# Kernel optimization log

Hardware: AMD Instinct MI355X
Metric: run time of the kernel (lower is better)

Reference implementation:

```python
import jax, jax.numpy as jnp
import numpy as np

N, E, IN_DIM, OUT_DIM, R = 50000, 800000, 128, 128, 8


def setup_inputs() -> dict:
    key = jax.random.key(0)
    k1, k2, k3, k4, k5 = jax.random.split(key, 5)
    x = jax.random.normal(k1, (N, IN_DIM), dtype=jnp.float32)
    edge_index = jax.random.randint(k2, (2, E), 0, N, dtype=jnp.int32)
    edge_type = jax.random.randint(k3, (E,), 0, R, dtype=jnp.int32)
    # Xavier-uniform-ish init for parameters
    lim_w = float(np.sqrt(6.0 / (IN_DIM + OUT_DIM)))
    weight = jax.random.uniform(k4, (R, IN_DIM, OUT_DIM), dtype=jnp.float32, minval=-lim_w, maxval=lim_w)
    self_weight = jax.random.uniform(k5, (IN_DIM, OUT_DIM), dtype=jnp.float32, minval=-lim_w, maxval=lim_w)
    return {"x": x, "weight": weight, "self_weight": self_weight,
            "edge_index": edge_index, "edge_type": edge_type}


def reference(x, weight, self_weight, edge_index, edge_type):
    n = x.shape[0]
    r = weight.shape[0]
    d_out = weight.shape[2]
    src, dst = edge_index[0], edge_index[1]
    # undirected: symmetrize edges (directed=False)
    src_all = jnp.concatenate([src, dst])          # [2E]
    dst_all = jnp.concatenate([dst, src])          # [2E]
    et_all = jnp.concatenate([edge_type, edge_type])  # [2E]
    # transform all nodes by every relation weight once: [R, N, D_out]
    xw = jnp.einsum('ni,rio->rno', x, weight)
    # gather per-edge messages already transformed by their relation's W_r
    msg = xw[et_all, src_all]                      # [2E, D_out]
    # fused (relation, dst) segment id -> per-relation scatter-add
    seg = et_all.astype(jnp.int32) * n + dst_all
    agg = jax.ops.segment_sum(msg, seg, num_segments=r * n).reshape(r, n, d_out)
    deg = jax.ops.segment_sum(jnp.ones_like(seg, dtype=x.dtype), seg,
                              num_segments=r * n).reshape(r, n)
    deg_inv = jnp.where(deg > 0, 1.0 / jnp.maximum(deg, 1.0), jnp.zeros_like(deg))
    out = jnp.sum(agg * deg_inv[..., None], axis=0)  # [N, D_out]
    out = out + x @ self_weight                       # self-loop
    return out
```

## Files before the change

kernel.cpp:

```cpp
#include <hip/hip_runtime.h>

#define NN 50000
#define EE 800000
#define RR 8
#define DD 128
#define SS (NN*RR)
#define TE (2*EE)
#define NB 782
#define NBLK 391
#define NS (NB*NBLK)
#define CONVB 6826
#define XWB 391

typedef __attribute__((ext_vector_type(8))) short bf16x8;
typedef __attribute__((ext_vector_type(4))) float f32x4;

#define DRAIN_VM do { \
    asm volatile("s_waitcnt vmcnt(0)" ::: "memory"); \
    __builtin_amdgcn_sched_barrier(0); \
  } while (0)

__device__ __forceinline__ unsigned short f2bf(float f){
  unsigned int u = __float_as_uint(f);
  u += 0x7fffu + ((u >> 16) & 1u);
  return (unsigned short)(u >> 16);
}
__device__ __forceinline__ float bf_lo(unsigned int w){ return __uint_as_float(w << 16); }
__device__ __forceinline__ float bf_hi(unsigned int w){ return __uint_as_float(w & 0xffff0000u); }

__device__ __forceinline__ void acc8(float* a, uint4 u){
  a[0] += bf_lo(u.x); a[1] += bf_hi(u.x);
  a[2] += bf_lo(u.y); a[3] += bf_hi(u.y);
  a[4] += bf_lo(u.z); a[5] += bf_hi(u.z);
  a[6] += bf_lo(u.w); a[7] += bf_hi(u.w);
}
__device__ __forceinline__ void acc8s(float* a, uint4 u, float s){
  a[0] += s*bf_lo(u.x); a[1] += s*bf_hi(u.x);
  a[2] += s*bf_lo(u.y); a[3] += s*bf_hi(u.y);
  a[4] += s*bf_lo(u.z); a[5] += s*bf_hi(u.z);
  a[6] += s*bf_lo(u.w); a[7] += s*bf_hi(u.w);
}

__device__ __forceinline__ void dir_edge(const int* ei, const int* et, int j,
                                         int& s, int& d, int& t){
  if (j < EE){ s = ei[j]; d = ei[EE + j]; t = et[j]; }
  else { int jj = j - EE; s = ei[EE + jj]; d = ei[jj]; t = et[jj]; }
}

__global__ __launch_bounds__(256) void k_histconv(
    const int* __restrict__ ei, const int* __restrict__ et,
    int* __restrict__ hist,
    const float* __restrict__ x, const float* __restrict__ w,
    const float* __restrict__ sw,
    unsigned short* __restrict__ xb, unsigned short* __restrict__ wb)
{
  __shared__ int h[NB];
  if (blockIdx.x < NBLK){
    int tid = threadIdx.x, bid = blockIdx.x;
    for (int i = tid; i < NB; i += 256) h[i] = 0;
    __syncthreads();
    int j0 = bid*4096;
    for (int k = tid; k < 4096; k += 256){
      int j = j0 + k;
      if (j < TE){
        int d = (j < EE) ? ei[EE + j] : ei[j - EE];
        atomicAdd(&h[d >> 6], 1);
      }
    }
    __syncthreads();
    for (int i = tid; i < NB; i += 256) hist[i*NBLK + bid] = h[i];
  } else {
    int i = (blockIdx.x - NBLK)*256 + threadIdx.x;
    const int M1 = NN*DD/4;
    if (i < M1){
      float4 v = ((const float4*)x)[i];
      ushort4 o;
      o.x = f2bf(v.x); o.y = f2bf(v.y); o.z = f2bf(v.z); o.w = f2bf(v.w);
      ((ushort4*)xb)[i] = o;
    } else {
      int j = i - M1;
      if (j < 9*DD*DD){
        int r = j >> 14; int rem = j & 16383; int n = rem >> 7; int k = rem & 127;
        float v = (r < 8) ? w[r*16384 + k*128 + n] : sw[k*128 + n];
        wb[j] = f2bf(v);
      }
    }
  }
}

__global__ __launch_bounds__(256) void k_scan1(int* __restrict__ hist,
                                               int* __restrict__ blksum){
  __shared__ int sd[256];
  int b = blockIdx.x, tid = threadIdx.x;
  int base = b*1024 + tid*4;
  int v0 = (base+0 < NS) ? hist[base+0] : 0;
  int v1 = (base+1 < NS) ? hist[base+1] : 0;
  int v2 = (base+2 < NS) ? hist[base+2] : 0;
  int v3 = (base+3 < NS) ? hist[base+3] : 0;
  int ts = v0+v1+v2+v3;
  sd[tid] = ts; __syncthreads();
  for (int o = 1; o < 256; o <<= 1){
    int t = (tid >= o) ? sd[tid-o] : 0;
    __syncthreads();
    sd[tid] += t;
    __syncthreads();
  }
  int ex = sd[tid] - ts;
  if (base+0 < NS) hist[base+0] = ex; ex += v0;
  if (base+1 < NS) hist[base+1] = ex; ex += v1;
  if (base+2 < NS) hist[base+2] = ex; ex += v2;
  if (base+3 < NS) hist[base+3] = ex;
  if (tid == 255) blksum[b] = sd[255];
}

__global__ __launch_bounds__(256) void k_scan3(int* __restrict__ hist,
                                               const int* __restrict__ blksum){
  __shared__ int sd[256];
  int b = blockIdx.x, tid = threadIdx.x;
  int chunk = b >> 2;
  int s = 0;
  if (tid < chunk)       s  = blksum[tid];
  if (tid + 256 < chunk) s += blksum[tid + 256];
  sd[tid] = s; __syncthreads();
  for (int o = 128; o > 0; o >>= 1){
    if (tid < o) sd[tid] += sd[tid + o];
    __syncthreads();
  }
  int i = b*256 + tid;
  if (i < NS) hist[i] += sd[0];
}

__global__ __launch_bounds__(256, 4) void k_partxw(
    const int* __restrict__ ei, const int* __restrict__ et,
    const int* __restrict__ S, unsigned int* __restrict__ P,
    const unsigned short* __restrict__ xb,
    const unsigned short* __restrict__ wb,
    unsigned short* __restrict__ xw)
{
  __shared__ __align__(16) unsigned short Bs[2][8192];
  if (blockIdx.x < NBLK){
    int* cur = (int*)&Bs[0][0];
    int tid = threadIdx.x, bid = blockIdx.x;
    for (int i = tid; i < NB; i += 256) cur[i] = S[i*NBLK + bid];
    __syncthreads();
    int j0 = bid*4096;
    for (int k = tid; k < 4096; k += 256){
      int j = j0 + k;
      if (j < TE){
        int s, d, t; dir_edge(ei, et, j, s, d, t);
        int b2 = d >> 6;
        int p = atomicAdd(&cur[b2], 1);
        P[p] = (unsigned int)s | ((unsigned int)(d & 63) << 17)
             | ((unsigned int)t << 23);
      }
    }
  } else {
    const int bid  = blockIdx.x - NBLK;
    const int tid  = threadIdx.x;
    const int wave = tid >> 6, lane = tid & 63;
    const int l15  = lane & 15, quad = lane >> 4;
    const int row0 = bid * 128 + wave * 32;

    bf16x8 af[2][4];
    #pragma unroll
    for (int m = 0; m < 2; ++m){
      int gr = row0 + m*16 + l15; if (gr >= NN) gr = NN - 1;
      #pragma unroll
      for (int ks = 0; ks < 4; ++ks)
        af[m][ks] = *(const bf16x8*)(xb + (size_t)gr*DD + ks*32 + quad*8);
    }

    auto stage = [&](int rr, int hh, int bfb){
      #pragma unroll
      for (int j = 0; j < 4; ++j){
        int rowh = wave*16 + j*4 + (lane >> 4);
        int n = hh*64 + rowh;
        int c = lane & 15;
        const unsigned short* gp = wb + rr*16384 + n*128 + ((c ^ (n & 7)) << 3);
        __builtin_amdgcn_global_load_lds(
            (const __attribute__((address_space(1))) void*)gp,
            (__attribute__((address_space(3))) void*)((char*)&Bs[0][0] + bfb*16384 + wave*4096 + j*1024),
            16, 0, 0);
      }
    };

    stage(0, 0, 0);

    #pragma unroll 1
    for (int r = 0; r < 9; ++r){
      unsigned short* xs = xw + (size_t)r * NN * DD;
      #pragma unroll
      for (int u = 0; u < 2; ++u){
        DRAIN_VM;
        __syncthreads();
        int t = r*2 + u;
        if (t + 1 < 18) stage((t + 1) >> 1, (t + 1) & 1, (u + 1) & 1);
        const char* bb = (const char*)&Bs[0][0] + u*16384;
        #pragma unroll
        for (int lnt = 0; lnt < 4; ++lnt){
          int nt = u*4 + lnt;
          bf16x8 bf4[4];
          #pragma unroll
          for (int ks = 0; ks < 4; ++ks)
            bf4[ks] = *(const bf16x8*)(bb + (lnt*16 + l15)*256
                                          + (((ks*4 + quad) ^ (l15 & 7)) << 4));
          f32x4 C0 = (f32x4)(0.f), C1 = (f32x4)(0.f);
          #pragma unroll
          for (int ks = 0; ks < 4; ++ks){
            C0 = __builtin_amdgcn_mfma_f32_16x16x32_bf16(af[0][ks], bf4[ks], C0, 0, 0, 0);
            C1 = __builtin_amdgcn_mfma_f32_16x16x32_bf16(af[1][ks], bf4[ks], C1, 0, 0, 0);
          }
          #pragma unroll
          for (int i = 0; i < 4; ++i){
            int gr0 = row0 + quad*4 + i;
            int gr1 = row0 + 16 + quad*4 + i;
            if (gr0 < NN) xs[(size_t)gr0*DD + nt*16 + l15] = f2bf(C0[i]);
            if (gr1 < NN) xs[(size_t)gr1*DD + nt*16 + l15] = f2bf(C1[i]);
          }
        }
      }
    }
  }
}

__global__ __launch_bounds__(256) void k_build(const unsigned int* __restrict__ P,
                                               const int* __restrict__ S,
                                               int* __restrict__ esrc,
                                               int* __restrict__ offs){
  __shared__ int h[512], cu[512], sd[256];
  int tid = threadIdx.x, b = blockIdx.x;
  int pstart = S[b*NBLK];
  int pend   = (b+1 < NB) ? S[(b+1)*NBLK] : TE;
  int ne = pend - pstart;
  h[2*tid] = 0; h[2*tid+1] = 0;
  __syncthreads();
  for (int k = tid; k < ne; k += 256){
    unsigned int u = P[pstart + k];
    int lseg = (int)(((u >> 17) & 63u)*8u + (u >> 23));
    atomicAdd(&h[lseg], 1);
  }
  __syncthreads();
  int v0 = h[2*tid], v1 = h[2*tid+1];
  int ts = v0 + v1;
  sd[tid] = ts; __syncthreads();
  for (int o = 1; o < 256; o <<= 1){
    int t = (tid >= o) ? sd[tid-o] : 0;
    __syncthreads();
    sd[tid] += t;
    __syncthreads();
  }
  int ex = sd[tid] - ts;
  cu[2*tid]   = pstart + ex;
  cu[2*tid+1] = pstart + ex + v0;
  int seg0 = b*512;
  if (seg0 + 2*tid     < SS) offs[seg0 + 2*tid]     = cu[2*tid];
  if (seg0 + 2*tid + 1 < SS) offs[seg0 + 2*tid + 1] = cu[2*tid+1];
  if (b == NB-1 && tid == 0) offs[SS] = TE;
  __syncthreads();
  for (int k = tid; k < ne; k += 256){
    unsigned int u = P[pstart + k];
    int lseg = (int)(((u >> 17) & 63u)*8u + (u >> 23));
    int r = atomicAdd(&cu[lseg], 1);
    esrc[r] = (int)(u & 0x1ffffu) | (int)(((u >> 23) & 7u) << 17);
  }
}

__global__ __launch_bounds__(256, 4) void k_agg(
    const unsigned short* __restrict__ xw,
    const int* __restrict__ offs,
    const int* __restrict__ esrc,
    float* __restrict__ out)
{
  const int tid   = threadIdx.x;
  const int lane  = tid & 63;
  const int gl    = lane & 15;
  const int basel = lane & 48;
  const int d     = blockIdx.x * 16 + (tid >> 4);

  int o = 0;
  if (gl < 9) o = offs[d*8 + gl];
  int onx = __shfl(o, (basel + gl + 1) & 63);
  int cnt = onx - o;
  float scale = (gl < 8 && cnt > 0) ? 1.0f/(float)cnt : 0.0f;
  int ebase = __shfl(o, basel);
  int etot  = __shfl(o, basel + 8) - ebase;

  float a[8] = {0.f,0.f,0.f,0.f,0.f,0.f,0.f,0.f};

  int pk[8];
  #pragma unroll
  for (int s = 0; s < 8; ++s) pk[s] = (s < etot) ? esrc[ebase + s] : 0;

  for (int e = 0; e < etot; e += 8){
    uint4 U[8]; float sc[8];
    #pragma unroll
    for (int s = 0; s < 8; ++s){
      sc[s] = 0.f;
      U[s] = make_uint4(0u,0u,0u,0u);
      if (e + s < etot){
        int rel = (pk[s] >> 17) & 7;
        sc[s]   = __shfl(scale, basel + rel);
        int src = pk[s] & 0x1ffff;
        U[s] = *(const uint4*)(xw + ((size_t)rel*NN + src)*DD + gl*8);
      }
    }
    #pragma unroll
    for (int s = 0; s < 8; ++s){
      int en = e + 8 + s;
      pk[s] = (en < etot) ? esrc[ebase + en] : 0;
    }
    #pragma unroll
    for (int s = 0; s < 8; ++s) acc8s(a, U[s], sc[s]);
  }

  {
    uint4 u = *(const uint4*)(xw + ((size_t)8*NN + d)*DD + gl*8);
    acc8(a, u);
  }

  float4 v0; v0.x = a[0]; v0.y = a[1]; v0.z = a[2]; v0.w = a[3];
  float4 v1; v1.x = a[4]; v1.y = a[5]; v1.z = a[6]; v1.w = a[7];
  *(float4*)(out + (size_t)d*DD + gl*8)     = v0;
  *(float4*)(out + (size_t)d*DD + gl*8 + 4) = v1;
}

extern "C" void kernel_launch(void* const* d_in, const int* in_sizes, int n_in,
                              void* d_out, int out_size, void* d_ws, size_t ws_size,
                              hipStream_t stream){
  const float* x  = (const float*)d_in[0];
  const float* w  = (const float*)d_in[1];
  const float* sw = (const float*)d_in[2];
  const int*   ei = (const int*)d_in[3];
  const int*   et = (const int*)d_in[4];
  float* out = (float*)d_out;
  char* ws = (char*)d_ws;

  if (ws_size < (size_t)136295168) return;

  unsigned short* xb = (unsigned short*)(ws + 0);
  int*          esrc = (int*)(ws + 12800000);
  int*          offs = (int*)(ws + 19200000);
  unsigned short* wb = (unsigned short*)(ws + 20800016);
  unsigned short* xw = (unsigned short*)(ws + 21095168);

  unsigned int*    P = (unsigned int*)((char*)d_out + 0);
  int*          hist = (int*)((char*)d_out + 6400000);
  int*        blksum = (int*)((char*)d_out + 7623168);

  k_histconv<<<NBLK + CONVB, 256, 0, stream>>>(ei, et, hist, x, w, sw, xb, wb);
  k_scan1<<<(NS + 1023)/1024, 256, 0, stream>>>(hist, blksum);
  k_scan3<<<(NS + 255)/256, 256, 0, stream>>>(hist, blksum);
  k_partxw<<<NBLK + XWB, 256, 0, stream>>>(ei, et, hist, P, xb, wb, xw);
  k_build<<<NB, 256, 0, stream>>>(P, hist, esrc, offs);
  k_agg<<<NN/16, 256, 0, stream>>>(xw, offs, esrc, out);
}
```

Before: 228.8 us.

## Replace per-block histogram scan with global bucket totals and atomic cursors

```diff
diff --git a/kernel.cpp b/kernel.cpp
--- a/kernel.cpp
+++ b/kernel.cpp
@@ -8,7 +8,6 @@
 #define TE (2*EE)
 #define NB 782
 #define NBLK 391
-#define NS (NB*NBLK)
 #define CONVB 6826
 #define XWB 391
 
@@ -49,12 +48,15 @@
 
 __global__ __launch_bounds__(256) void k_histconv(
     const int* __restrict__ ei, const int* __restrict__ et,
-    int* __restrict__ hist,
+    int* __restrict__ btot, int* __restrict__ ticket,
+    int* __restrict__ bases, int* __restrict__ cursors,
     const float* __restrict__ x, const float* __restrict__ w,
     const float* __restrict__ sw,
     unsigned short* __restrict__ xb, unsigned short* __restrict__ wb)
 {
   __shared__ int h[NB];
+  __shared__ int sd[256];
+  __shared__ int lastflag;
   if (blockIdx.x < NBLK){
     int tid = threadIdx.x, bid = blockIdx.x;
     for (int i = tid; i < NB; i += 256) h[i] = 0;
@@ -68,7 +70,40 @@
       }
     }
     __syncthreads();
-    for (int i = tid; i < NB; i += 256) hist[i*NBLK + bid] = h[i];
+    for (int i = tid; i < NB; i += 256){
+      int c = h[i];
+      if (c) atomicAdd(&btot[i], c);
+    }
+    __threadfence();
+    __syncthreads();
+    if (tid == 0){
+      int old = atomicAdd(ticket, 1);
+      lastflag = (old == NBLK - 1);
+    }
+    __syncthreads();
+    if (lastflag){
+      for (int i = tid; i < NB; i += 256) h[i] = atomicAdd(&btot[i], 0);
+      __syncthreads();
+      int base4 = tid*4;
+      int v0 = (base4+0 < NB) ? h[base4+0] : 0;
+      int v1 = (base4+1 < NB) ? h[base4+1] : 0;
+      int v2 = (base4+2 < NB) ? h[base4+2] : 0;
+      int v3 = (base4+3 < NB) ? h[base4+3] : 0;
+      int ts = v0+v1+v2+v3;
+      sd[tid] = ts; __syncthreads();
+      for (int o = 1; o < 256; o <<= 1){
+        int t = (tid >= o) ? sd[tid-o] : 0;
+        __syncthreads();
+        sd[tid] += t;
+        __syncthreads();
+      }
+      int ex = sd[tid] - ts;
+      if (base4+0 < NB){ bases[base4+0] = ex; cursors[base4+0] = ex; } ex += v0;
+      if (base4+1 < NB){ bases[base4+1] = ex; cursors[base4+1] = ex; } ex += v1;
+      if (base4+2 < NB){ bases[base4+2] = ex; cursors[base4+2] = ex; } ex += v2;
+      if (base4+3 < NB){ bases[base4+3] = ex; cursors[base4+3] = ex; }
+      if (tid == 0) bases[NB] = TE;
+    }
   } else {
     int i = (blockIdx.x - NBLK)*256 + threadIdx.x;
     const int M1 = NN*DD/4;
@@ -88,51 +123,9 @@
   }
 }
 
-__global__ __launch_bounds__(256) void k_scan1(int* __restrict__ hist,
-                                               int* __restrict__ blksum){
-  __shared__ int sd[256];
-  int b = blockIdx.x, tid = threadIdx.x;
-  int base = b*1024 + tid*4;
-  int v0 = (base+0 < NS) ? hist[base+0] : 0;
-  int v1 = (base+1 < NS) ? hist[base+1] : 0;
-  int v2 = (base+2 < NS) ? hist[base+2] : 0;
-  int v3 = (base+3 < NS) ? hist[base+3] : 0;
-  int ts = v0+v1+v2+v3;
-  sd[tid] = ts; __syncthreads();
-  for (int o = 1; o < 256; o <<= 1){
-    int t = (tid >= o) ? sd[tid-o] : 0;
-    __syncthreads();
-    sd[tid] += t;
-    __syncthreads();
-  }
-  int ex = sd[tid] - ts;
-  if (base+0 < NS) hist[base+0] = ex; ex += v0;
-  if (base+1 < NS) hist[base+1] = ex; ex += v1;
-  if (base+2 < NS) hist[base+2] = ex; ex += v2;
-  if (base+3 < NS) hist[base+3] = ex;
-  if (tid == 255) blksum[b] = sd[255];
-}
-
-__global__ __launch_bounds__(256) void k_scan3(int* __restrict__ hist,
-                                               const int* __restrict__ blksum){
-  __shared__ int sd[256];
-  int b = blockIdx.x, tid = threadIdx.x;
-  int chunk = b >> 2;
-  int s = 0;
-  if (tid < chunk)       s  = blksum[tid];
-  if (tid + 256 < chunk) s += blksum[tid + 256];
-  sd[tid] = s; __syncthreads();
-  for (int o = 128; o > 0; o >>= 1){
-    if (tid < o) sd[tid] += sd[tid + o];
-    __syncthreads();
-  }
-  int i = b*256 + tid;
-  if (i < NS) hist[i] += sd[0];
-}
-
 __global__ __launch_bounds__(256, 4) void k_partxw(
     const int* __restrict__ ei, const int* __restrict__ et,
-    const int* __restrict__ S, unsigned int* __restrict__ P,
+    int* __restrict__ cursors, unsigned int* __restrict__ P,
     const unsigned short* __restrict__ xb,
     const unsigned short* __restrict__ wb,
     unsigned short* __restrict__ xw)
@@ -141,17 +134,36 @@
   if (blockIdx.x < NBLK){
     int* cur = (int*)&Bs[0][0];
     int tid = threadIdx.x, bid = blockIdx.x;
-    for (int i = tid; i < NB; i += 256) cur[i] = S[i*NBLK + bid];
+    for (int i = tid; i < NB; i += 256) cur[i] = 0;
     __syncthreads();
     int j0 = bid*4096;
-    for (int k = tid; k < 4096; k += 256){
-      int j = j0 + k;
+    unsigned int pkreg[16]; int bkreg[16];
+    #pragma unroll
+    for (int k16 = 0; k16 < 16; ++k16){
+      int j = j0 + k16*256 + tid;
+      int b2 = -1; unsigned int pv = 0u;
       if (j < TE){
         int s, d, t; dir_edge(ei, et, j, s, d, t);
-        int b2 = d >> 6;
-        int p = atomicAdd(&cur[b2], 1);
-        P[p] = (unsigned int)s | ((unsigned int)(d & 63) << 17)
-             | ((unsigned int)t << 23);
+        b2 = d >> 6;
+        pv = (unsigned int)s | ((unsigned int)(d & 63) << 17)
+           | ((unsigned int)t << 23);
+        atomicAdd(&cur[b2], 1);
+      }
+      pkreg[k16] = pv; bkreg[k16] = b2;
+    }
+    __syncthreads();
+    for (int i = tid; i < NB; i += 256){
+      int c = cur[i];
+      int base = 0;
+      if (c) base = atomicAdd(&cursors[i], c);
+      cur[i] = base;
+    }
+    __syncthreads();
+    #pragma unroll
+    for (int k16 = 0; k16 < 16; ++k16){
+      if (bkreg[k16] >= 0){
+        int p = atomicAdd(&cur[bkreg[k16]], 1);
+        P[p] = pkreg[k16];
       }
     }
   } else {
@@ -224,13 +236,13 @@
 }
 
 __global__ __launch_bounds__(256) void k_build(const unsigned int* __restrict__ P,
-                                               const int* __restrict__ S,
+                                               const int* __restrict__ bases,
                                                int* __restrict__ esrc,
                                                int* __restrict__ offs){
   __shared__ int h[512], cu[512], sd[256];
   int tid = threadIdx.x, b = blockIdx.x;
-  int pstart = S[b*NBLK];
-  int pend   = (b+1 < NB) ? S[(b+1)*NBLK] : TE;
+  int pstart = bases[b];
+  int pend   = bases[b+1];
   int ne = pend - pstart;
   h[2*tid] = 0; h[2*tid+1] = 0;
   __syncthreads();
@@ -344,13 +356,15 @@
   unsigned short* xw = (unsigned short*)(ws + 21095168);
 
   unsigned int*    P = (unsigned int*)((char*)d_out + 0);
-  int*          hist = (int*)((char*)d_out + 6400000);
-  int*        blksum = (int*)((char*)d_out + 7623168);
-
-  k_histconv<<<NBLK + CONVB, 256, 0, stream>>>(ei, et, hist, x, w, sw, xb, wb);
-  k_scan1<<<(NS + 1023)/1024, 256, 0, stream>>>(hist, blksum);
-  k_scan3<<<(NS + 255)/256, 256, 0, stream>>>(hist, blksum);
-  k_partxw<<<NBLK + XWB, 256, 0, stream>>>(ei, et, hist, P, xb, wb, xw);
-  k_build<<<NB, 256, 0, stream>>>(P, hist, esrc, offs);
+  int*          btot = (int*)((char*)d_out + 6400000);
+  int*        ticket = (int*)((char*)d_out + 6403128);
+  int*         bases = (int*)((char*)d_out + 6403200);
+  int*       cursors = (int*)((char*)d_out + 6406400);
+
+  hipMemsetAsync(btot, 0, 3132, stream);
+  k_histconv<<<NBLK + CONVB, 256, 0, stream>>>(ei, et, btot, ticket,
+                                               bases, cursors, x, w, sw, xb, wb);
+  k_partxw<<<NBLK + XWB, 256, 0, stream>>>(ei, et, cursors, P, xb, wb, xw);
+  k_build<<<NB, 256, 0, stream>>>(P, bases, esrc, offs);
   k_agg<<<NN/16, 256, 0, stream>>>(xw, offs, esrc, out);
 }
```

After: 246.4 us. +7.7%, slower.
